# Performance work log

Measured on AMD Instinct MI355X. Metric: run time of the kernel, lower is better.

The kernel has to match this reference:

```python
import jax, jax.numpy as jnp
import numpy as np

H = 512
B, LQ, LA = 16, 64, 100


def setup_inputs() -> dict:
    key = jax.random.key(0)
    ks = jax.random.split(key, 10)
    s = 1.0 / np.sqrt(H)
    return {
        "content1": jax.random.normal(ks[0], (B, LQ, H), dtype=jnp.float32),
        "content2": jax.random.normal(ks[1], (B, LA, H), dtype=jnp.float32),
        "is_user": 0,
        "W_q": jax.random.normal(ks[2], (H, H), dtype=jnp.float32) * s,
        "b_q": jax.random.normal(ks[3], (H,), dtype=jnp.float32) * s,
        "W_a": jax.random.normal(ks[4], (H, H), dtype=jnp.float32) * s,
        "b_a": jax.random.normal(ks[5], (H,), dtype=jnp.float32) * s,
        "W_aq": jax.random.normal(ks[6], (H, H), dtype=jnp.float32) * s,
        "b_aq": jax.random.normal(ks[7], (H,), dtype=jnp.float32) * s,
        "W_v": jax.random.normal(ks[8], (H, 1), dtype=jnp.float32) * s,
        "b_v": jax.random.normal(ks[9], (1,), dtype=jnp.float32) * s,
    }


def _entropy(x, axis):
    logp = jax.nn.log_softmax(x, axis=axis)
    p = jnp.exp(logp)
    return -1.0 * jnp.sum(p * logp, axis=axis)


def reference(content1, content2, is_user, W_q, b_q, W_a, b_a, W_aq, b_aq, W_v, b_v):
    # Branch is_user==0 (question x answer mutual attention).
    # Original expands content1 to [B,Lq,La,H] and content2 to [B,Lq,La,H];
    # since the three linears are applied to values constant along the
    # broadcast axes, we project pre-expansion (same math, less FLOPs).
    # m = tanh(w_a_m(c1) + w_q_m(c2) + w_aq_m(c1*c1))  (c1*c1 as in source)
    a1 = content1 @ W_a + b_a + (content1 * content1) @ W_aq + b_aq  # [B,Lq,H]
    q2 = content2 @ W_q + b_q                                        # [B,La,H]
    m = jnp.tanh(a1[:, :, None, :] + q2[:, None, :, :])              # [B,Lq,La,H]
    score = m @ W_v + b_v                                            # [B,Lq,La,1]
    beta = _entropy(score, axis=2)                                   # [B,Lq,1]
    return beta
```

## Files before the change

kernel.cpp:

```cpp
#include <hip/hip_runtime.h>
#include <math.h>

#define H    512
#define LQ   64
#define LA   100
#define LAP  128
#define L2E2 2.885390081777927f

using short8  = __attribute__((ext_vector_type(8))) short;
using floatx4 = __attribute__((ext_vector_type(4))) float;

__device__ __forceinline__ unsigned short f2bf(float f) {
    unsigned int u = __float_as_uint(f);
    u += 0x7fffu + ((u >> 16) & 1u);
    return (unsigned short)(u >> 16);
}
__device__ __forceinline__ unsigned int packbf2(float a, float b) {
    return (unsigned int)f2bf(a) | ((unsigned int)f2bf(b) << 16);
}

__device__ __forceinline__ void async_cp16(const void* g, void* l) {
    __builtin_amdgcn_global_load_lds(
        (const __attribute__((address_space(1))) unsigned int*)(uintptr_t)g,
        (__attribute__((address_space(3))) unsigned int*)(unsigned int)(uintptr_t)l,
        16, 0, 0);
}

__global__ __launch_bounds__(256) void prep_kernel(
    const float* __restrict__ c1, const float* __restrict__ c2,
    const float* __restrict__ Wq, const float* __restrict__ Wa,
    const float* __restrict__ Waq,
    unsigned short* __restrict__ A1sw, unsigned short* __restrict__ A2sw,
    unsigned short* __restrict__ B1sw, unsigned short* __restrict__ B2sw)
{
    __shared__ __align__(16) float lt[64][68];
    const int bid = blockIdx.x, t = threadIdx.x;

    if (bid < 328) {
        const bool isA1 = bid < 128;
        int mt, kc; const float* X;
        if (isA1) { mt = bid >> 3; kc = bid & 7; X = c1; }
        else      { int b2 = bid - 128; mt = b2 >> 3; kc = b2 & 7; X = c2; }
#pragma unroll
        for (int i = 0; i < 4; ++i) {
            int idx = i * 256 + t;
            int r = idx >> 4, c4 = idx & 15;
            float4 v = *(const float4*)(X + (size_t)(mt * 64 + r) * H + kc * 64 + c4 * 4);
            int bytepos = r * 128 + (((c4 >> 1) ^ (r & 7)) * 16) + (c4 & 1) * 8;
            if (isA1) {
                unsigned short* t1 = A1sw + (size_t)(mt * 16 + kc) * 4096;
                *(uint2*)((char*)t1 + bytepos) = make_uint2(packbf2(v.x, v.y), packbf2(v.z, v.w));
                unsigned short* t2 = A1sw + (size_t)(mt * 16 + kc + 8) * 4096;
                *(uint2*)((char*)t2 + bytepos) =
                    make_uint2(packbf2(v.x * v.x, v.y * v.y), packbf2(v.z * v.z, v.w * v.w));
            } else {
                unsigned short* t1 = A2sw + (size_t)(mt * 8 + kc) * 4096;
                *(uint2*)((char*)t1 + bytepos) = make_uint2(packbf2(v.x, v.y), packbf2(v.z, v.w));
            }
        }
    } else {
        int b3 = bid - 328;
        const bool isB1 = b3 < 128;
        int nt, kc; const float* W; int k0;
        if (isB1) { nt = b3 >> 4; kc = b3 & 15; W = (kc < 8) ? Wa : Waq; k0 = (kc & 7) * 64; }
        else      { int b4 = b3 - 128; nt = b4 >> 3; kc = b4 & 7; W = Wq; k0 = kc * 64; }
        const int n0 = nt * 64;
#pragma unroll
        for (int i = 0; i < 4; ++i) {
            int idx = i * 256 + t;
            int k = idx >> 4, n4 = idx & 15;
            float4 v = *(const float4*)(W + (size_t)(k0 + k) * H + n0 + n4 * 4);
            lt[n4 * 4 + 0][k] = v.x;
            lt[n4 * 4 + 1][k] = v.y;
            lt[n4 * 4 + 2][k] = v.z;
            lt[n4 * 4 + 3][k] = v.w;
        }
        __syncthreads();
#pragma unroll
        for (int i = 0; i < 4; ++i) {
            int idx = i * 256 + t;
            int r = idx >> 4, c4 = idx & 15;
            float4 v = *(const float4*)&lt[r][c4 * 4];
            int bytepos = r * 128 + (((c4 >> 1) ^ (r & 7)) * 16) + (c4 & 1) * 8;
            unsigned short* tile = isB1 ? B1sw + (size_t)(nt * 16 + kc) * 4096
                                        : B2sw + (size_t)(nt * 8 + kc) * 4096;
            *(uint2*)((char*)tile + bytepos) = make_uint2(packbf2(v.x, v.y), packbf2(v.z, v.w));
        }
    }
}

__global__ __launch_bounds__(256) void gemm_kernel(
    const unsigned short* __restrict__ A1sw, const unsigned short* __restrict__ A2sw,
    const unsigned short* __restrict__ B1sw, const unsigned short* __restrict__ B2sw,
    const float* __restrict__ bq, const float* __restrict__ ba,
    const float* __restrict__ baq,
    float* __restrict__ a1, float* __restrict__ q2t)
{
    __shared__ __align__(16) unsigned short As[2][4096];
    __shared__ __align__(16) unsigned short Bs[2][4096];

    const int bid = blockIdx.x;
    const bool g1 = bid < 128;
    int mt, nt, nk;
    const unsigned short *Abase, *Bbase;
    if (g1) {
        mt = bid >> 3; nt = bid & 7; nk = 16;
        Abase = A1sw + (size_t)(mt * 16) * 4096;
        Bbase = B1sw + (size_t)(nt * 16) * 4096;
    } else {
        int b2 = bid - 128; mt = b2 >> 3; nt = b2 & 7; nk = 8;
        Abase = A2sw + (size_t)(mt * 8) * 4096;
        Bbase = B2sw + (size_t)(nt * 8) * 4096;
    }
    const int m0 = mt * 64, n0 = nt * 64;

    const int t = threadIdx.x;
    const int w = t >> 6, lane = t & 63;
    const int q = lane >> 4, ln = lane & 15;
    const int goff = w * 1024 + lane * 8;
    const int loff = w * 1024;

    floatx4 acc[4];
#pragma unroll
    for (int j = 0; j < 4; ++j) acc[j] = (floatx4){0.f, 0.f, 0.f, 0.f};

    {
        const unsigned short* ga = Abase;
        const unsigned short* gb = Bbase;
        async_cp16(ga + goff,       &As[0][loff]);
        async_cp16(ga + goff + 512, &As[0][loff + 512]);
        async_cp16(gb + goff,       &Bs[0][loff]);
        async_cp16(gb + goff + 512, &Bs[0][loff + 512]);
    }
    __syncthreads();

    int buf = 0;
    for (int kc = 0; kc < nk; ++kc) {
        if (kc + 1 < nk) {
            const unsigned short* ga = Abase + (size_t)(kc + 1) * 4096;
            const unsigned short* gb = Bbase + (size_t)(kc + 1) * 4096;
            async_cp16(ga + goff,       &As[buf ^ 1][loff]);
            async_cp16(ga + goff + 512, &As[buf ^ 1][loff + 512]);
            async_cp16(gb + goff,       &Bs[buf ^ 1][loff]);
            async_cp16(gb + goff + 512, &Bs[buf ^ 1][loff + 512]);
        }
#pragma unroll
        for (int s = 0; s < 2; ++s) {
            const int off = ((s * 4 + q) ^ (ln & 7)) * 16;
            short8 af = *(const short8*)((const char*)&As[buf][0] + (w * 16 + ln) * 128 + off);
#pragma unroll
            for (int j = 0; j < 4; ++j) {
                short8 bf = *(const short8*)((const char*)&Bs[buf][0] + (j * 16 + ln) * 128 + off);
                acc[j] = __builtin_amdgcn_mfma_f32_16x16x32_bf16(af, bf, acc[j], 0, 0, 0);
            }
        }
        __syncthreads();
        buf ^= 1;
    }

    if (g1) {
#pragma unroll
        for (int j = 0; j < 4; ++j) {
            const int N = n0 + j * 16 + ln;
            const float bias = ba[N] + baq[N];
#pragma unroll
            for (int r = 0; r < 4; ++r) {
                const int R = m0 + w * 16 + q * 4 + r;
                a1[(size_t)R * H + N] = (acc[j][r] + bias) * L2E2;
            }
        }
    } else {
#pragma unroll
        for (int r = 0; r < 4; ++r) {
            const int R = m0 + w * 16 + q * 4 + r;
            const int bb = (R * 5243) >> 19;
            const int aa = R - bb * 100;
            float* dst = q2t + (size_t)bb * (H * LAP) + aa;
#pragma unroll
            for (int j = 0; j < 4; ++j) {
                const int N = n0 + j * 16 + ln;
                dst[(size_t)N * LAP] = (acc[j][r] + bq[N]) * L2E2;
            }
        }
    }
}

__global__ __launch_bounds__(1024) void score_entropy_kernel(
    const float* __restrict__ a1, const float* __restrict__ q2t,
    const float* __restrict__ wvp, const float* __restrict__ bvp,
    float* __restrict__ out)
{
    __shared__ __align__(16) float a1s[4][H];
    __shared__ __align__(16) float wvs[H];
    __shared__ __align__(16) float part[8][LAP][4];

    const int t  = threadIdx.x;
    const int b  = blockIdx.x >> 4;
    const int qg = blockIdx.x & 15;

    for (int i = t; i < 4 * H; i += 1024) {
        int q = i >> 9, h = i & (H - 1);
        a1s[q][h] = a1[(size_t)(b * LQ + (qg << 2) + q) * H + h];
    }
    if (t < H) wvs[t] = wvp[t];
    __syncthreads();

    const int a  = t & 127;
    const int hh = t >> 7;
    const int hb = hh * 64;
    const float* q2p = q2t + (size_t)b * (H * LAP) + (size_t)hb * LAP + a;

    float R0 = 0.f, R1 = 0.f, R2 = 0.f, R3 = 0.f;
#define TERM(Rq, Aq, vv, ww) \
    Rq = fmaf(ww, __builtin_amdgcn_rcpf(__builtin_amdgcn_exp2f((Aq) + (vv)) + 1.f), Rq)
#pragma unroll 4
    for (int i = 0; i < 16; ++i) {
        const int h4 = i * 4;
        float4 wv4 = *(const float4*)&wvs[hb + h4];
        float4 A0 = *(const float4*)&a1s[0][hb + h4];
        float4 A1 = *(const float4*)&a1s[1][hb + h4];
        float4 A2 = *(const float4*)&a1s[2][hb + h4];
        float4 A3 = *(const float4*)&a1s[3][hb + h4];
        float v0 = q2p[(size_t)(h4 + 0) * LAP];
        float v1 = q2p[(size_t)(h4 + 1) * LAP];
        float v2 = q2p[(size_t)(h4 + 2) * LAP];
        float v3 = q2p[(size_t)(h4 + 3) * LAP];
        TERM(R0, A0.x, v0, wv4.x); TERM(R0, A0.y, v1, wv4.y);
        TERM(R0, A0.z, v2, wv4.z); TERM(R0, A0.w, v3, wv4.w);
        TERM(R1, A1.x, v0, wv4.x); TERM(R1, A1.y, v1, wv4.y);
        TERM(R1, A1.z, v2, wv4.z); TERM(R1, A1.w, v3, wv4.w);
        TERM(R2, A2.x, v0, wv4.x); TERM(R2, A2.y, v1, wv4.y);
        TERM(R2, A2.z, v2, wv4.z); TERM(R2, A2.w, v3, wv4.w);
        TERM(R3, A3.x, v0, wv4.x); TERM(R3, A3.y, v1, wv4.y);
        TERM(R3, A3.z, v2, wv4.z); TERM(R3, A3.w, v3, wv4.w);
    }
#undef TERM
    *(float4*)(&part[hh][a][0]) = make_float4(R0, R1, R2, R3);
    __syncthreads();

    if (t < 256) {
        const int l = t & 63, q = t >> 6;
        float ws = 0.f;
#pragma unroll
        for (int i = 0; i < 8; ++i) ws += wvs[l + (i << 6)];
#pragma unroll
        for (int o = 32; o; o >>= 1) ws += __shfl_xor(ws, o);

        const float base = bvp[0] + ws;
        float s1 = 0.f, s2 = 0.f;
#pragma unroll
        for (int i = 0; i < 8; ++i) s1 += part[i][l][q];
        const bool act2 = l < (LA - 64);
        if (act2) {
#pragma unroll
            for (int i = 0; i < 8; ++i) s2 += part[i][l + 64][q];
        }
        float sc1 = base - 2.f * s1;
        float sc2 = act2 ? (base - 2.f * s2) : -INFINITY;
        float m = fmaxf(sc1, sc2);
#pragma unroll
        for (int o = 32; o; o >>= 1) m = fmaxf(m, __shfl_xor(m, o));

        const float L2E = 1.4426950408889634f;
        float e1 = __builtin_amdgcn_exp2f((sc1 - m) * L2E);
        float e2 = act2 ? __builtin_amdgcn_exp2f((sc2 - m) * L2E) : 0.f;
        float Z = e1 + e2;
        float S = e1 * sc1 + (act2 ? e2 * sc2 : 0.f);
#pragma unroll
        for (int o = 32; o; o >>= 1) {
            Z += __shfl_xor(Z, o);
            S += __shfl_xor(S, o);
        }
        if (l == 0) out[b * LQ + (qg << 2) + q] = m + logf(Z) - S / Z;
    }
}

extern "C" void kernel_launch(void* const* d_in, const int* in_sizes, int n_in,
                              void* d_out, int out_size, void* d_ws, size_t ws_size,
                              hipStream_t stream) {
    const float* c1  = (const float*)d_in[0];
    const float* c2  = (const float*)d_in[1];
    const float* Wq  = (const float*)d_in[3];
    const float* bq  = (const float*)d_in[4];
    const float* Wa  = (const float*)d_in[5];
    const float* ba  = (const float*)d_in[6];
    const float* Waq = (const float*)d_in[7];
    const float* baq = (const float*)d_in[8];
    const float* Wv  = (const float*)d_in[9];
    const float* bv  = (const float*)d_in[10];
    float* out = (float*)d_out;

    float* a1  = (float*)d_ws;
    float* q2t = a1 + (size_t)1024 * 512;
    unsigned short* A1sw = (unsigned short*)(q2t + (size_t)16 * 512 * 128);
    unsigned short* A2sw = A1sw + (size_t)16 * 16 * 4096;
    unsigned short* B1sw = A2sw + (size_t)25 * 8 * 4096;
    unsigned short* B2sw = B1sw + (size_t)8 * 16 * 4096;

    prep_kernel<<<dim3(520), dim3(256), 0, stream>>>(c1, c2, Wq, Wa, Waq,
                                                     A1sw, A2sw, B1sw, B2sw);
    gemm_kernel<<<dim3(328), dim3(256), 0, stream>>>(A1sw, A2sw, B1sw, B2sw,
                                                     bq, ba, baq, a1, q2t);
    score_entropy_kernel<<<dim3(256), dim3(1024), 0, stream>>>(a1, q2t, Wv, bv, out);
}
```

Measured before the change: 105.9 us.

## Load GEMM fragments directly from global and enlarge c2 projection tiles

The GEMM kernel stops staging A/B tiles through double-buffered LDS with async copies and barriers. Each wave now reads its bf16 MFMA fragments straight from the pre-swizzled global buffers. The c2 projection GEMM moves to 128-row tiles with two accumulator sets per wave, which cuts its block count and reuses each B fragment twice. This removes LDS traffic and syncs but relies on L2/L1 for reuse across waves. The padded 26th A2 tile is read but never written by prep, so its rows are masked in the epilogue.

Measured after the change: 109.0 us. 1.03x slower.

```diff
diff --git a/kernel.cpp b/kernel.cpp
--- a/kernel.cpp
+++ b/kernel.cpp
@@ -17,13 +17,6 @@
 }
 __device__ __forceinline__ unsigned int packbf2(float a, float b) {
     return (unsigned int)f2bf(a) | ((unsigned int)f2bf(b) << 16);
-}
-
-__device__ __forceinline__ void async_cp16(const void* g, void* l) {
-    __builtin_amdgcn_global_load_lds(
-        (const __attribute__((address_space(1))) unsigned int*)(uintptr_t)g,
-        (__attribute__((address_space(3))) unsigned int*)(unsigned int)(uintptr_t)l,
-        16, 0, 0);
 }
 
 __global__ __launch_bounds__(256) void prep_kernel(
@@ -96,69 +89,37 @@
     const float* __restrict__ baq,
     float* __restrict__ a1, float* __restrict__ q2t)
 {
-    __shared__ __align__(16) unsigned short As[2][4096];
-    __shared__ __align__(16) unsigned short Bs[2][4096];
-
-    const int bid = blockIdx.x;
-    const bool g1 = bid < 128;
-    int mt, nt, nk;
-    const unsigned short *Abase, *Bbase;
-    if (g1) {
-        mt = bid >> 3; nt = bid & 7; nk = 16;
-        Abase = A1sw + (size_t)(mt * 16) * 4096;
-        Bbase = B1sw + (size_t)(nt * 16) * 4096;
-    } else {
-        int b2 = bid - 128; mt = b2 >> 3; nt = b2 & 7; nk = 8;
-        Abase = A2sw + (size_t)(mt * 8) * 4096;
-        Bbase = B2sw + (size_t)(nt * 8) * 4096;
-    }
-    const int m0 = mt * 64, n0 = nt * 64;
-
-    const int t = threadIdx.x;
-    const int w = t >> 6, lane = t & 63;
-    const int q = lane >> 4, ln = lane & 15;
-    const int goff = w * 1024 + lane * 8;
-    const int loff = w * 1024;
-
-    floatx4 acc[4];
-#pragma unroll
-    for (int j = 0; j < 4; ++j) acc[j] = (floatx4){0.f, 0.f, 0.f, 0.f};
-
-    {
-        const unsigned short* ga = Abase;
-        const unsigned short* gb = Bbase;
-        async_cp16(ga + goff,       &As[0][loff]);
-        async_cp16(ga + goff + 512, &As[0][loff + 512]);
-        async_cp16(gb + goff,       &Bs[0][loff]);
-        async_cp16(gb + goff + 512, &Bs[0][loff + 512]);
-    }
-    __syncthreads();
-
-    int buf = 0;
-    for (int kc = 0; kc < nk; ++kc) {
-        if (kc + 1 < nk) {
-            const unsigned short* ga = Abase + (size_t)(kc + 1) * 4096;
-            const unsigned short* gb = Bbase + (size_t)(kc + 1) * 4096;
-            async_cp16(ga + goff,       &As[buf ^ 1][loff]);
-            async_cp16(ga + goff + 512, &As[buf ^ 1][loff + 512]);
-            async_cp16(gb + goff,       &Bs[buf ^ 1][loff]);
-            async_cp16(gb + goff + 512, &Bs[buf ^ 1][loff + 512]);
-        }
-#pragma unroll
-        for (int s = 0; s < 2; ++s) {
-            const int off = ((s * 4 + q) ^ (ln & 7)) * 16;
-            short8 af = *(const short8*)((const char*)&As[buf][0] + (w * 16 + ln) * 128 + off);
-#pragma unroll
-            for (int j = 0; j < 4; ++j) {
-                short8 bf = *(const short8*)((const char*)&Bs[buf][0] + (j * 16 + ln) * 128 + off);
-                acc[j] = __builtin_amdgcn_mfma_f32_16x16x32_bf16(af, bf, acc[j], 0, 0, 0);
-            }
-        }
-        __syncthreads();
-        buf ^= 1;
-    }
-
-    if (g1) {
+    const int bid  = blockIdx.x;
+    const int t    = threadIdx.x;
+    const int w    = t >> 6, lane = t & 63;
+    const int q    = lane >> 4, ln = lane & 15;
+
+    if (bid < 128) {
+        const int mt = bid >> 3, nt = bid & 7;
+        const char* Ab = (const char*)(A1sw + (size_t)(mt * 16) * 4096)
+                         + (w * 16 + ln) * 128;
+        const char* Bb = (const char*)(B1sw + (size_t)(nt * 16) * 4096)
+                         + ln * 128;
+        floatx4 acc[4];
+#pragma unroll
+        for (int j = 0; j < 4; ++j) acc[j] = (floatx4){0.f, 0.f, 0.f, 0.f};
+
+#pragma unroll 2
+        for (int kc = 0; kc < 16; ++kc) {
+            const char* ga = Ab + kc * 8192;
+            const char* gb = Bb + kc * 8192;
+#pragma unroll
+            for (int s = 0; s < 2; ++s) {
+                const int off = ((s * 4 + q) ^ (ln & 7)) * 16;
+                short8 af = *(const short8*)(ga + off);
+#pragma unroll
+                for (int j = 0; j < 4; ++j) {
+                    short8 bf = *(const short8*)(gb + j * 2048 + off);
+                    acc[j] = __builtin_amdgcn_mfma_f32_16x16x32_bf16(af, bf, acc[j], 0, 0, 0);
+                }
+            }
+        }
+        const int m0 = mt * 64, n0 = nt * 64;
 #pragma unroll
         for (int j = 0; j < 4; ++j) {
             const int N = n0 + j * 16 + ln;
@@ -170,16 +131,52 @@
             }
         }
     } else {
-#pragma unroll
-        for (int r = 0; r < 4; ++r) {
-            const int R = m0 + w * 16 + q * 4 + r;
-            const int bb = (R * 5243) >> 19;
-            const int aa = R - bb * 100;
-            float* dst = q2t + (size_t)bb * (H * LAP) + aa;
-#pragma unroll
-            for (int j = 0; j < 4; ++j) {
-                const int N = n0 + j * 16 + ln;
-                dst[(size_t)N * LAP] = (acc[j][r] + bq[N]) * L2E2;
+        const int b2 = bid - 128;
+        const int mt = b2 >> 3, nt = b2 & 7;
+        const int tile64 = mt * 2 + (w >> 1);
+        const char* A0p = (const char*)(A2sw + (size_t)(tile64 * 8) * 4096)
+                          + ((w & 1) * 32 + ln) * 128;
+        const char* A1p = A0p + 16 * 128;
+        const char* Bb  = (const char*)(B2sw + (size_t)(nt * 8) * 4096)
+                          + ln * 128;
+        floatx4 acc[2][4];
+#pragma unroll
+        for (int rh = 0; rh < 2; ++rh)
+#pragma unroll
+            for (int j = 0; j < 4; ++j) acc[rh][j] = (floatx4){0.f, 0.f, 0.f, 0.f};
+
+#pragma unroll 2
+        for (int kc = 0; kc < 8; ++kc) {
+            const char* gb = Bb + kc * 8192;
+#pragma unroll
+            for (int s = 0; s < 2; ++s) {
+                const int off = ((s * 4 + q) ^ (ln & 7)) * 16;
+                short8 af0 = *(const short8*)(A0p + kc * 8192 + off);
+                short8 af1 = *(const short8*)(A1p + kc * 8192 + off);
+#pragma unroll
+                for (int j = 0; j < 4; ++j) {
+                    short8 bf = *(const short8*)(gb + j * 2048 + off);
+                    acc[0][j] = __builtin_amdgcn_mfma_f32_16x16x32_bf16(af0, bf, acc[0][j], 0, 0, 0);
+                    acc[1][j] = __builtin_amdgcn_mfma_f32_16x16x32_bf16(af1, bf, acc[1][j], 0, 0, 0);
+                }
+            }
+        }
+        const int n0 = nt * 64;
+#pragma unroll
+        for (int rh = 0; rh < 2; ++rh) {
+#pragma unroll
+            for (int r = 0; r < 4; ++r) {
+                const int R = mt * 128 + w * 32 + rh * 16 + q * 4 + r;
+                if (R < 1600) {
+                    const int bb = (R * 5243) >> 19;
+                    const int aa = R - bb * 100;
+                    float* dst = q2t + (size_t)bb * (H * LAP) + aa;
+#pragma unroll
+                    for (int j = 0; j < 4; ++j) {
+                        const int N = n0 + j * 16 + ln;
+                        dst[(size_t)N * LAP] = (acc[rh][j][r] + bq[N]) * L2E2;
+                    }
+                }
             }
         }
     }
@@ -294,12 +291,12 @@
     float* q2t = a1 + (size_t)1024 * 512;
     unsigned short* A1sw = (unsigned short*)(q2t + (size_t)16 * 512 * 128);
     unsigned short* A2sw = A1sw + (size_t)16 * 16 * 4096;
-    unsigned short* B1sw = A2sw + (size_t)25 * 8 * 4096;
+    unsigned short* B1sw = A2sw + (size_t)26 * 8 * 4096;
     unsigned short* B2sw = B1sw + (size_t)8 * 16 * 4096;
 
     prep_kernel<<<dim3(520), dim3(256), 0, stream>>>(c1, c2, Wq, Wa, Waq,
                                                      A1sw, A2sw, B1sw, B2sw);
-    gemm_kernel<<<dim3(328), dim3(256), 0, stream>>>(A1sw, A2sw, B1sw, B2sw,
+    gemm_kernel<<<dim3(232), dim3(256), 0, stream>>>(A1sw, A2sw, B1sw, B2sw,
                                                      bq, ba, baq, a1, q2t);
     score_entropy_kernel<<<dim3(256), dim3(1024), 0, stream>>>(a1, q2t, Wv, bv, out);
 }
```
